# Kernel tuning notes

Measured on AMD Instinct MI355X. Metric: run time of the kernel, lower is better.

## Reference

```python
import jax, jax.numpy as jnp
import numpy as np

N = 50000      # nodes
E = 800000     # edges (avg in-degree 16)
IN_DIM = 128
OUT_DIM = 64
LEAKY_SLOPE = 0.01  # torch F.leaky_relu default


def setup_inputs() -> dict:
    key = jax.random.key(0)
    ks = jax.random.split(key, 7)
    h = jax.random.normal(ks[0], (N, IN_DIM), dtype=jnp.float32)
    r_h = jax.random.normal(ks[1], (E, OUT_DIM), dtype=jnp.float32)
    edge_src = jax.random.randint(ks[2], (E,), 0, N, dtype=jnp.int32)
    edge_dst = jax.random.randint(ks[3], (E,), 0, N, dtype=jnp.int32)
    # learned params (xavier-ish scaling)
    W_fc = jax.random.normal(ks[4], (OUT_DIM, IN_DIM), dtype=jnp.float32) * (1.0 / np.sqrt(IN_DIM))
    attn_w = jax.random.normal(ks[5], (1, 3 * OUT_DIM), dtype=jnp.float32) * 0.1
    loop_weight = jax.random.normal(ks[6], (OUT_DIM, OUT_DIM), dtype=jnp.float32) * (1.0 / np.sqrt(OUT_DIM))
    return {"h": h, "r_h": r_h, "W_fc": W_fc, "attn_w": attn_w,
            "loop_weight": loop_weight, "edge_src": edge_src, "edge_dst": edge_dst}


def reference(h, r_h, W_fc, attn_w, loop_weight, edge_src, edge_dst):
    # z = fc(h)   [N, OUT_DIM]
    z = h @ W_fc.T
    z_src = z[edge_src]          # [E, OUT_DIM]
    z_dst = z[edge_dst]          # [E, OUT_DIM]
    # attn_fc(cat([z_src, z_dst, r_h])) expressed without materializing the concat
    w1 = attn_w[0, :OUT_DIM]
    w2 = attn_w[0, OUT_DIM:2 * OUT_DIM]
    w3 = attn_w[0, 2 * OUT_DIM:]
    a = z_src @ w1 + z_dst @ w2 + r_h @ w3            # [E]
    e = jax.nn.leaky_relu(a, LEAKY_SLOPE)
    # segment softmax over incoming edges of each destination node
    seg_max = jax.ops.segment_max(e, edge_dst, num_segments=N)  # -inf for deg-0 (never gathered)
    e_exp = jnp.exp(e - jax.lax.stop_gradient(seg_max)[edge_dst])
    denom = jax.ops.segment_sum(e_exp, edge_dst, num_segments=N)
    alpha = e_exp / denom[edge_dst]                   # [E]
    # weighted scatter-sum of source features
    agg = jax.ops.segment_sum(alpha[:, None] * z_src, edge_dst, num_segments=N)  # [N, OUT_DIM]
    # DGL only runs reduce_func (incl. self-loop matmul) on nodes with in-edges
    deg = jax.ops.segment_sum(jnp.ones((E,), jnp.float32), edge_dst, num_segments=N)
    h_out = jnp.where(deg[:, None] > 0, agg + z @ loop_weight, 0.0)
    return jax.nn.relu(h_out)
```

## Files before the change

### kernel.cpp

```cpp
#include <hip/hip_runtime.h>
#include <hip/hip_bf16.h>

#define NN 50000
#define EE 800000
#define IND 128
#define OUTD 64
#define NB 49
#define PA_BLOCKS 782
#define DEG_BLOCKS 391
#define RH_BLOCKS 6250

__global__ __launch_bounds__(256) void k_front(
    const float* __restrict__ h, const float* __restrict__ W,
    const float* __restrict__ attn, const int* __restrict__ edst,
    const float* __restrict__ r_h,
    __hip_bfloat16* __restrict__ zb, float* __restrict__ s1,
    float* __restrict__ s2, int* __restrict__ deg, int* __restrict__ rank,
    float* __restrict__ d3) {
  const int tid = threadIdx.x;
  if (blockIdx.x >= PA_BLOCKS + DEG_BLOCKS) {
    const int base4 = (blockIdx.x - (PA_BLOCKS + DEG_BLOCKS)) * 2048 + tid;
    const int sub = tid & 15;
    const float4 wv = reinterpret_cast<const float4*>(attn + 2 * OUTD)[sub];
    float4 rv[8];
#pragma unroll
    for (int j = 0; j < 8; ++j)
      rv[j] = reinterpret_cast<const float4*>(r_h)[base4 + j * 256];
    float d[8];
#pragma unroll
    for (int j = 0; j < 8; ++j)
      d[j] = rv[j].x * wv.x + rv[j].y * wv.y + rv[j].z * wv.z + rv[j].w * wv.w;
#pragma unroll
    for (int m = 1; m <= 8; m <<= 1) {
#pragma unroll
      for (int j = 0; j < 8; ++j) d[j] += __shfl_xor(d[j], m, 64);
    }
    if (sub == 0) {
      const int row0 = base4 >> 4;
#pragma unroll
      for (int j = 0; j < 8; ++j) d3[row0 + 16 * j] = d[j];
    }
    return;
  }
  if (blockIdx.x >= PA_BLOCKS) {
    const int base = (blockIdx.x - PA_BLOCKS) * 2048 + tid;
#pragma unroll
    for (int j = 0; j < 8; ++j) {
      int e = base + j * 256;
      if (e < EE) rank[e] = atomicAdd(&deg[edst[e]], 1);
    }
    return;
  }
  __shared__ float Wl[64 * 129];
#pragma unroll
  for (int j = 0; j < 8; ++j) {
    int i4 = tid + j * 256;
    const float4 v = reinterpret_cast<const float4*>(W)[i4];
    int i = i4 * 4;
    int col = i >> 7, k = i & 127;
    float* p = &Wl[col * 129 + k];
    p[0] = v.x; p[1] = v.y; p[2] = v.z; p[3] = v.w;
  }
  __syncthreads();
  const int lane = tid & 63;
  const int wid = tid >> 6;
  float Wreg[128];
#pragma unroll
  for (int k = 0; k < 128; ++k) Wreg[k] = Wl[lane * 129 + k];
  const float w1v = attn[lane];
  const float w2v = attn[64 + lane];
  const int base = blockIdx.x * 64 + wid * 16;
  for (int i = 0; i < 16; ++i) {
    int r = base + i;
    if (r >= NN) return;
    const float* hr = h + (size_t)r * IND;
    float h0 = hr[lane];
    float h1 = hr[64 + lane];
    float a0 = 0.f, a1 = 0.f, a2 = 0.f, a3 = 0.f;
#pragma unroll
    for (int k = 0; k < 16; ++k) {
      a0 = fmaf(__uint_as_float(__builtin_amdgcn_readlane(__float_as_uint(h0), 4 * k)),     Wreg[4 * k], a0);
      a1 = fmaf(__uint_as_float(__builtin_amdgcn_readlane(__float_as_uint(h0), 4 * k + 1)), Wreg[4 * k + 1], a1);
      a2 = fmaf(__uint_as_float(__builtin_amdgcn_readlane(__float_as_uint(h0), 4 * k + 2)), Wreg[4 * k + 2], a2);
      a3 = fmaf(__uint_as_float(__builtin_amdgcn_readlane(__float_as_uint(h0), 4 * k + 3)), Wreg[4 * k + 3], a3);
    }
#pragma unroll
    for (int k = 0; k < 16; ++k) {
      a0 = fmaf(__uint_as_float(__builtin_amdgcn_readlane(__float_as_uint(h1), 4 * k)),     Wreg[64 + 4 * k], a0);
      a1 = fmaf(__uint_as_float(__builtin_amdgcn_readlane(__float_as_uint(h1), 4 * k + 1)), Wreg[64 + 4 * k + 1], a1);
      a2 = fmaf(__uint_as_float(__builtin_amdgcn_readlane(__float_as_uint(h1), 4 * k + 2)), Wreg[64 + 4 * k + 2], a2);
      a3 = fmaf(__uint_as_float(__builtin_amdgcn_readlane(__float_as_uint(h1), 4 * k + 3)), Wreg[64 + 4 * k + 3], a3);
    }
    float acc = (a0 + a1) + (a2 + a3);
    zb[(size_t)r * OUTD + lane] = __float2bfloat16(acc);
    float p = acc * w1v, q = acc * w2v;
#pragma unroll
    for (int m = 32; m >= 1; m >>= 1) {
      p += __shfl_xor(p, m, 64);
      q += __shfl_xor(q, m, 64);
    }
    if (lane == 0) { s1[r] = p; s2[r] = q; }
  }
}

__global__ __launch_bounds__(1024) void k_scan1(
    const int* __restrict__ deg, int* __restrict__ offL,
    int* __restrict__ blocksum) {
  __shared__ int wsum[16];
  __shared__ int woff[17];
  const int tid = threadIdx.x;
  const int gid = blockIdx.x * 1024 + tid;
  const int lane = tid & 63, wid = tid >> 6;
  int v = (gid < NN) ? deg[gid] : 0;
  int incl = v;
#pragma unroll
  for (int o = 1; o < 64; o <<= 1) {
    int t = __shfl_up(incl, o, 64);
    if (lane >= o) incl += t;
  }
  if (lane == 63) wsum[wid] = incl;
  __syncthreads();
  if (wid == 0 && lane < 16) {
    int s = wsum[lane];
    int si = s;
#pragma unroll
    for (int o = 1; o < 16; o <<= 1) {
      int t = __shfl_up(si, o, 64);
      if (lane >= o) si += t;
    }
    woff[lane] = si - s;
    if (lane == 15) woff[16] = si;
  }
  __syncthreads();
  if (gid < NN) offL[gid] = woff[wid] + incl - v;
  if (tid == 0) blocksum[blockIdx.x] = woff[16];
}

__global__ __launch_bounds__(64) void k_scan2(
    const int* __restrict__ blocksum, int* __restrict__ blockoff) {
  const int lane = threadIdx.x;
  int v = (lane < NB) ? blocksum[lane] : 0;
  int incl = v;
#pragma unroll
  for (int o = 1; o < 64; o <<= 1) {
    int t = __shfl_up(incl, o, 64);
    if (lane >= o) incl += t;
  }
  if (lane < NB) blockoff[lane] = incl - v;
}

__global__ __launch_bounds__(256) void k_scatter(
    const int* __restrict__ esrc, const int* __restrict__ edst,
    const float* __restrict__ d3, const float* __restrict__ s1,
    const float* __restrict__ s2, const int* __restrict__ rank,
    const int* __restrict__ offL, const int* __restrict__ blockoff,
    int2* __restrict__ pairs) {
  const int e = blockIdx.x * 256 + threadIdx.x;
  if (e >= EE) return;
  int s = esrc[e], dd = edst[e];
  float a = s1[s] + s2[dd] + d3[e];
  float el = a > 0.f ? a : 0.01f * a;
  float ex = __expf(el);
  int pos = blockoff[dd >> 10] + offL[dd] + rank[e];
  pairs[pos] = make_int2(s, __float_as_int(ex));
}

__global__ __launch_bounds__(256) void k_agg(
    const __hip_bfloat16* __restrict__ zb, const int2* __restrict__ pairs,
    const int* __restrict__ offL, const int* __restrict__ blockoff,
    const int* __restrict__ deg, const float* __restrict__ LW,
    float* __restrict__ out) {
  const int lane = threadIdx.x & 63, wid = threadIdx.x >> 6;
  const int slot = lane >> 4, sub = lane & 15;
  float4 LWreg[16];
#pragma unroll
  for (int kl = 0; kl < 16; ++kl)
    LWreg[kl] = reinterpret_cast<const float4*>(LW)[(slot * 16 + kl) * 16 + sub];
  const int r = blockIdx.x * 4 + wid;
  const int cnt = deg[r];
  const int2* pp = pairs + (blockoff[r >> 10] + offL[r]);
  float4 acc = make_float4(0.f, 0.f, 0.f, 0.f);
  float wsum = 0.f;
  for (int i = 0; i < cnt; i += 16) {
    int2 p[4];
    float w[4];
#pragma unroll
    for (int j = 0; j < 4; ++j) {
      int e = i + j * 4 + slot;
      bool v = e < cnt;
      p[j] = pp[v ? e : 0];
      w[j] = v ? __int_as_float(p[j].y) : 0.f;
    }
#pragma unroll
    for (int j = 0; j < 4; ++j) {
      ushort4 uz = reinterpret_cast<const ushort4*>(zb)[(size_t)p[j].x * 16 + sub];
      acc.x = fmaf(w[j], __uint_as_float((unsigned)uz.x << 16), acc.x);
      acc.y = fmaf(w[j], __uint_as_float((unsigned)uz.y << 16), acc.y);
      acc.z = fmaf(w[j], __uint_as_float((unsigned)uz.z << 16), acc.z);
      acc.w = fmaf(w[j], __uint_as_float((unsigned)uz.w << 16), acc.w);
      wsum += w[j];
    }
  }
  float4 lacc = make_float4(0.f, 0.f, 0.f, 0.f);
#pragma unroll
  for (int j = 0; j < 4; ++j) {
    ushort4 uz = reinterpret_cast<const ushort4*>(zb)[(size_t)r * 16 + slot * 4 + j];
    float zk[4] = {__uint_as_float((unsigned)uz.x << 16),
                   __uint_as_float((unsigned)uz.y << 16),
                   __uint_as_float((unsigned)uz.z << 16),
                   __uint_as_float((unsigned)uz.w << 16)};
#pragma unroll
    for (int c = 0; c < 4; ++c) {
      float4 lw = LWreg[4 * j + c];
      lacc.x = fmaf(zk[c], lw.x, lacc.x);
      lacc.y = fmaf(zk[c], lw.y, lacc.y);
      lacc.z = fmaf(zk[c], lw.z, lacc.z);
      lacc.w = fmaf(zk[c], lw.w, lacc.w);
    }
  }
  wsum += __shfl_xor(wsum, 16, 64);
  wsum += __shfl_xor(wsum, 32, 64);
  float inv = (cnt > 0) ? 1.f / wsum : 0.f;
  float4 t;
  t.x = fmaf(acc.x, inv, lacc.x);
  t.y = fmaf(acc.y, inv, lacc.y);
  t.z = fmaf(acc.z, inv, lacc.z);
  t.w = fmaf(acc.w, inv, lacc.w);
  t.x += __shfl_xor(t.x, 16, 64); t.x += __shfl_xor(t.x, 32, 64);
  t.y += __shfl_xor(t.y, 16, 64); t.y += __shfl_xor(t.y, 32, 64);
  t.z += __shfl_xor(t.z, 16, 64); t.z += __shfl_xor(t.z, 32, 64);
  t.w += __shfl_xor(t.w, 16, 64); t.w += __shfl_xor(t.w, 32, 64);
  if (slot == 0) {
    float4 res;
    res.x = (cnt > 0 && t.x > 0.f) ? t.x : 0.f;
    res.y = (cnt > 0 && t.y > 0.f) ? t.y : 0.f;
    res.z = (cnt > 0 && t.z > 0.f) ? t.z : 0.f;
    res.w = (cnt > 0 && t.w > 0.f) ? t.w : 0.f;
    reinterpret_cast<float4*>(out)[(size_t)r * 16 + sub] = res;
  }
}

extern "C" void kernel_launch(void* const* d_in, const int* in_sizes, int n_in,
                              void* d_out, int out_size, void* d_ws, size_t ws_size,
                              hipStream_t stream) {
  const float* h    = (const float*)d_in[0];
  const float* r_h  = (const float*)d_in[1];
  const float* W_fc = (const float*)d_in[2];
  const float* attn = (const float*)d_in[3];
  const float* LW   = (const float*)d_in[4];
  const int* esrc   = (const int*)d_in[5];
  const int* edst   = (const int*)d_in[6];
  float* out = (float*)d_out;

  char* ws = (char*)d_ws;
  __hip_bfloat16* zb = (__hip_bfloat16*)(ws);
  int2*  pairs = (int2*)(ws + 6400000);
  int*   rank  = (int*)(ws + 12800000);
  float* d3    = (float*)(ws + 16000000);
  float* s1    = (float*)(ws + 19200000);
  float* s2    = (float*)(ws + 19400000);
  int*   deg   = (int*)(ws + 19600000);
  int*   offL  = (int*)(ws + 19800000);
  int*   bsum  = (int*)(ws + 20000000);
  int*   boff  = (int*)(ws + 20001024);

  hipMemsetAsync(deg, 0, (size_t)NN * sizeof(int), stream);

  k_front<<<PA_BLOCKS + DEG_BLOCKS + RH_BLOCKS, 256, 0, stream>>>(
      h, W_fc, attn, edst, r_h, zb, s1, s2, deg, rank, d3);
  k_scan1<<<NB, 1024, 0, stream>>>(deg, offL, bsum);
  k_scan2<<<1, 64, 0, stream>>>(bsum, boff);
  k_scatter<<<(EE + 255) / 256, 256, 0, stream>>>(
      esrc, edst, d3, s1, s2, rank, offL, boff, pairs);
  k_agg<<<NN / 4, 256, 0, stream>>>(zb, pairs, offL, boff, deg, LW, out);
}
```

Measured before the change: 422.5 us.

## Split front kernel into streaming and GEMM kernels, vectorize edge scatter

Splits the fused front kernel into a streaming kernel (degree counting plus r_h dot products) and a separate GEMM kernel with launch_bounds(256,1). The heavy-register GEMM path then no longer sets the occupancy of the light streaming blocks. The GEMM row loop now uses a precomputed row bound instead of an early return. The scatter kernel processes four edges per thread with int4/float4 loads to cut instruction and load overhead. The cost is one extra kernel launch and a serialization point between the two former halves.

```diff
diff --git a/kernel.cpp b/kernel.cpp
--- a/kernel.cpp
+++ b/kernel.cpp
@@ -10,40 +10,13 @@
 #define DEG_BLOCKS 391
 #define RH_BLOCKS 6250
 
-__global__ __launch_bounds__(256) void k_front(
-    const float* __restrict__ h, const float* __restrict__ W,
+__global__ __launch_bounds__(256) void k_stream(
     const float* __restrict__ attn, const int* __restrict__ edst,
-    const float* __restrict__ r_h,
-    __hip_bfloat16* __restrict__ zb, float* __restrict__ s1,
-    float* __restrict__ s2, int* __restrict__ deg, int* __restrict__ rank,
-    float* __restrict__ d3) {
+    const float* __restrict__ r_h, int* __restrict__ deg,
+    int* __restrict__ rank, float* __restrict__ d3) {
   const int tid = threadIdx.x;
-  if (blockIdx.x >= PA_BLOCKS + DEG_BLOCKS) {
-    const int base4 = (blockIdx.x - (PA_BLOCKS + DEG_BLOCKS)) * 2048 + tid;
-    const int sub = tid & 15;
-    const float4 wv = reinterpret_cast<const float4*>(attn + 2 * OUTD)[sub];
-    float4 rv[8];
-#pragma unroll
-    for (int j = 0; j < 8; ++j)
-      rv[j] = reinterpret_cast<const float4*>(r_h)[base4 + j * 256];
-    float d[8];
-#pragma unroll
-    for (int j = 0; j < 8; ++j)
-      d[j] = rv[j].x * wv.x + rv[j].y * wv.y + rv[j].z * wv.z + rv[j].w * wv.w;
-#pragma unroll
-    for (int m = 1; m <= 8; m <<= 1) {
-#pragma unroll
-      for (int j = 0; j < 8; ++j) d[j] += __shfl_xor(d[j], m, 64);
-    }
-    if (sub == 0) {
-      const int row0 = base4 >> 4;
-#pragma unroll
-      for (int j = 0; j < 8; ++j) d3[row0 + 16 * j] = d[j];
-    }
-    return;
-  }
-  if (blockIdx.x >= PA_BLOCKS) {
-    const int base = (blockIdx.x - PA_BLOCKS) * 2048 + tid;
+  if (blockIdx.x < DEG_BLOCKS) {
+    const int base = blockIdx.x * 2048 + tid;
 #pragma unroll
     for (int j = 0; j < 8; ++j) {
       int e = base + j * 256;
@@ -51,6 +24,34 @@
     }
     return;
   }
+  const int base4 = (blockIdx.x - DEG_BLOCKS) * 2048 + tid;
+  const int sub = tid & 15;
+  const float4 wv = reinterpret_cast<const float4*>(attn + 2 * OUTD)[sub];
+  float4 rv[8];
+#pragma unroll
+  for (int j = 0; j < 8; ++j)
+    rv[j] = reinterpret_cast<const float4*>(r_h)[base4 + j * 256];
+  float d[8];
+#pragma unroll
+  for (int j = 0; j < 8; ++j)
+    d[j] = rv[j].x * wv.x + rv[j].y * wv.y + rv[j].z * wv.z + rv[j].w * wv.w;
+#pragma unroll
+  for (int m = 1; m <= 8; m <<= 1) {
+#pragma unroll
+    for (int j = 0; j < 8; ++j) d[j] += __shfl_xor(d[j], m, 64);
+  }
+  if (sub == 0) {
+    const int row0 = base4 >> 4;
+#pragma unroll
+    for (int j = 0; j < 8; ++j) d3[row0 + 16 * j] = d[j];
+  }
+}
+
+__global__ __launch_bounds__(256, 1) void k_gemm(
+    const float* __restrict__ h, const float* __restrict__ W,
+    const float* __restrict__ attn, __hip_bfloat16* __restrict__ zb,
+    float* __restrict__ s1, float* __restrict__ s2) {
+  const int tid = threadIdx.x;
   __shared__ float Wl[64 * 129];
 #pragma unroll
   for (int j = 0; j < 8; ++j) {
@@ -70,9 +71,10 @@
   const float w1v = attn[lane];
   const float w2v = attn[64 + lane];
   const int base = blockIdx.x * 64 + wid * 16;
-  for (int i = 0; i < 16; ++i) {
+  int rmax = NN - base;
+  rmax = rmax > 16 ? 16 : (rmax < 0 ? 0 : rmax);
+  for (int i = 0; i < rmax; ++i) {
     int r = base + i;
-    if (r >= NN) return;
     const float* hr = h + (size_t)r * IND;
     float h0 = hr[lane];
     float h1 = hr[64 + lane];
@@ -155,14 +157,27 @@
     const float* __restrict__ s2, const int* __restrict__ rank,
     const int* __restrict__ offL, const int* __restrict__ blockoff,
     int2* __restrict__ pairs) {
-  const int e = blockIdx.x * 256 + threadIdx.x;
-  if (e >= EE) return;
-  int s = esrc[e], dd = edst[e];
-  float a = s1[s] + s2[dd] + d3[e];
-  float el = a > 0.f ? a : 0.01f * a;
-  float ex = __expf(el);
-  int pos = blockoff[dd >> 10] + offL[dd] + rank[e];
-  pairs[pos] = make_int2(s, __float_as_int(ex));
+  const int t = blockIdx.x * 256 + threadIdx.x;
+  if (t >= EE / 4) return;
+  const int4 s4 = reinterpret_cast<const int4*>(esrc)[t];
+  const int4 dd4 = reinterpret_cast<const int4*>(edst)[t];
+  const float4 d34 = reinterpret_cast<const float4*>(d3)[t];
+  const int4 rk4 = reinterpret_cast<const int4*>(rank)[t];
+  float v1x = s1[s4.x], v1y = s1[s4.y], v1z = s1[s4.z], v1w = s1[s4.w];
+  float v2x = s2[dd4.x], v2y = s2[dd4.y], v2z = s2[dd4.z], v2w = s2[dd4.w];
+  int oLx = offL[dd4.x], oLy = offL[dd4.y], oLz = offL[dd4.z], oLw = offL[dd4.w];
+  int bx = blockoff[dd4.x >> 10], by = blockoff[dd4.y >> 10];
+  int bz = blockoff[dd4.z >> 10], bw = blockoff[dd4.w >> 10];
+  float ax = v1x + v2x + d34.x, ay = v1y + v2y + d34.y;
+  float az = v1z + v2z + d34.z, aw = v1w + v2w + d34.w;
+  float ex = __expf(ax > 0.f ? ax : 0.01f * ax);
+  float ey = __expf(ay > 0.f ? ay : 0.01f * ay);
+  float ez = __expf(az > 0.f ? az : 0.01f * az);
+  float ew = __expf(aw > 0.f ? aw : 0.01f * aw);
+  pairs[bx + oLx + rk4.x] = make_int2(s4.x, __float_as_int(ex));
+  pairs[by + oLy + rk4.y] = make_int2(s4.y, __float_as_int(ey));
+  pairs[bz + oLz + rk4.z] = make_int2(s4.z, __float_as_int(ez));
+  pairs[bw + oLw + rk4.w] = make_int2(s4.w, __float_as_int(ew));
 }
 
 __global__ __launch_bounds__(256) void k_agg(
@@ -266,11 +281,12 @@
 
   hipMemsetAsync(deg, 0, (size_t)NN * sizeof(int), stream);
 
-  k_front<<<PA_BLOCKS + DEG_BLOCKS + RH_BLOCKS, 256, 0, stream>>>(
-      h, W_fc, attn, edst, r_h, zb, s1, s2, deg, rank, d3);
+  k_stream<<<DEG_BLOCKS + RH_BLOCKS, 256, 0, stream>>>(
+      attn, edst, r_h, deg, rank, d3);
+  k_gemm<<<PA_BLOCKS, 256, 0, stream>>>(h, W_fc, attn, zb, s1, s2);
   k_scan1<<<NB, 1024, 0, stream>>>(deg, offL, bsum);
   k_scan2<<<1, 64, 0, stream>>>(bsum, boff);
-  k_scatter<<<(EE + 255) / 256, 256, 0, stream>>>(
+  k_scatter<<<(EE / 4 + 255) / 256, 256, 0, stream>>>(
       esrc, edst, d3, s1, s2, rank, offL, boff, pairs);
   k_agg<<<NN / 4, 256, 0, stream>>>(zb, pairs, offL, boff, deg, LW, out);
 }
```

Measured after the change: 424.9 us. About the same (+0.6%).
